# Kernel optimization log

Measured on AMD Instinct MI355X. Metric: run time of the kernel, lower is better.

Reference implementation:

```python
import jax, jax.numpy as jnp
import numpy as np

N = 100000   # nodes
E = 1600000  # edges
F = 64       # num_features
H = 64       # hidden_units
C = 10       # num_classes
G = 1000     # graphs in batch
BN_EPS = 1e-5


def setup_inputs() -> dict:
    key = jax.random.key(0)
    ks = jax.random.split(key, 32)
    inp = {
        "x": jax.random.normal(ks[0], (N, F), dtype=jnp.float32),
        "edge_index": jax.random.randint(ks[1], (2, E), 0, N, dtype=jnp.int64),
        "batch": jnp.sort(jax.random.randint(ks[2], (N,), 0, G, dtype=jnp.int64)),
    }
    i = 3
    def w(shape, scale):
        nonlocal i
        a = jax.random.normal(ks[i], shape, dtype=jnp.float32) * scale
        i += 1
        return a
    for l, din in [(0, F), (1, H)]:
        inp[f"c{l}_w1"] = w((din, H), 1.0 / np.sqrt(din))
        inp[f"c{l}_b1"] = jnp.zeros((H,), jnp.float32)
        inp[f"c{l}_g1"] = jnp.ones((H,), jnp.float32)
        inp[f"c{l}_be1"] = jnp.zeros((H,), jnp.float32)
        inp[f"c{l}_w2"] = w((H, H), 1.0 / np.sqrt(H))
        inp[f"c{l}_b2"] = jnp.zeros((H,), jnp.float32)
        inp[f"bn{l}_g"] = jnp.ones((H,), jnp.float32)
        inp[f"bn{l}_b"] = jnp.zeros((H,), jnp.float32)
    for l, din in [(0, F), (1, H), (2, H)]:
        inp[f"l{l}_w"] = w((din, C), 1.0 / np.sqrt(din))
        inp[f"l{l}_b"] = jnp.zeros((C,), jnp.float32)
    return inp


def _bn(h, g, b):
    # BatchNorm1d in training mode: batch statistics over node axis
    m = jnp.mean(h, axis=0)
    v = jnp.var(h, axis=0)
    return g * (h - m) * jax.lax.rsqrt(v + BN_EPS) + b


def _gin_conv(h, src, dst, w1, b1, g1, be1, w2, b2):
    # scatter-add neighbor aggregation: out[dst] += h[src]; eps = 0
    agg = jax.ops.segment_sum(h[src], dst, num_segments=N)
    z = h + agg                      # (1 + eps) * x + sum_j x_j
    z = jax.nn.relu(_bn(z @ w1 + b1, g1, be1))
    return z @ w2 + b2


def reference(x, edge_index, batch,
              c0_w1, c0_b1, c0_g1, c0_be1, c0_w2, c0_b2, bn0_g, bn0_b,
              c1_w1, c1_b1, c1_g1, c1_be1, c1_w2, c1_b2, bn1_g, bn1_b,
              l0_w, l0_b, l1_w, l1_b, l2_w, l2_b):
    src, dst = edge_index[0], edge_index[1]
    h0 = x
    h1 = jax.nn.relu(_bn(_gin_conv(h0, src, dst, c0_w1, c0_b1, c0_g1, c0_be1, c0_w2, c0_b2), bn0_g, bn0_b))
    h2 = jax.nn.relu(_bn(_gin_conv(h1, src, dst, c1_w1, c1_b1, c1_g1, c1_be1, c1_w2, c1_b2), bn1_g, bn1_b))
    # jumping-knowledge readout: per-layer global_add_pool -> Linear -> sum (dropout=0)
    out = jnp.zeros((G, C), dtype=x.dtype)
    for h, w, b in [(h0, l0_w, l0_b), (h1, l1_w, l1_b), (h2, l2_w, l2_b)]:
        pooled = jax.ops.segment_sum(h, batch, num_segments=G)
        out = out + pooled @ w + b
    return out
```

## Files before the change

kernel.cpp:

```cpp
#include <hip/hip_runtime.h>
#include <hip/hip_bf16.h>

#define BN_EPS 1e-5f
#define NBMAX 512
#define CHUNK 4096
#define CAP   5120
#define PCAP  7168

typedef __hip_bfloat16 bf16;
typedef __attribute__((ext_vector_type(8))) short short8;
typedef __attribute__((ext_vector_type(4))) float f32x4;

__device__ __forceinline__ float b2f(bf16 v) { return __bfloat162float(v); }
__device__ __forceinline__ bf16 f2b(float v) { return __float2bfloat16(v); }
__device__ __forceinline__ float bl(unsigned u) { return __uint_as_float(u << 16); }
__device__ __forceinline__ float bh(unsigned u) { return __uint_as_float(u & 0xffff0000u); }
__device__ __forceinline__ unsigned pack2(float x, float y) {
    union { bf16 b[2]; unsigned u; } p;
    p.b[0] = f2b(x); p.b[1] = f2b(y);
    return p.u;
}
__device__ __forceinline__ float bs2f(short s) {
    return __uint_as_float(((unsigned)(unsigned short)s) << 16);
}
__device__ __forceinline__ short f2bs(float v) {
    bf16 b = f2b(v);
    return *reinterpret_cast<short*>(&b);
}

__global__ __launch_bounds__(256) void initcast_k(
    const float* __restrict__ in, bf16* __restrict__ out, int n4, int total4,
    int* __restrict__ bcur, int NB)
{
    if (blockIdx.x == 0) {
        for (int i = threadIdx.x; i < NB; i += 256) bcur[i] = i * CAP;
    }
    int i = blockIdx.x * 256 + threadIdx.x;
    if (i >= total4) return;
    if (i < n4) {
        float4 v = ((const float4*)in)[i];
        union { ushort4 u; bf16 b[4]; } p;
        p.b[0] = f2b(v.x); p.b[1] = f2b(v.y); p.b[2] = f2b(v.z); p.b[3] = f2b(v.w);
        ((ushort4*)out)[i] = p.u;
    } else {
        ushort4 z; z.x = 0; z.y = 0; z.z = 0; z.w = 0;
        ((ushort4*)out)[i] = z;
    }
}

__global__ __launch_bounds__(256) void binscatter_k(
    const int* __restrict__ src, const int* __restrict__ dst,
    int* __restrict__ bcur, int* __restrict__ tmp, int E, int NB)
{
    __shared__ int hist[NBMAX];
    __shared__ int loff[NBMAX];
    __shared__ int gb[NBMAX];
    __shared__ int lcur[NBMAX];
    __shared__ int staged[CHUNK];
    __shared__ unsigned short sb[CHUNK];
    __shared__ int ssc[256];
    const int t = threadIdx.x;
    for (int i = t; i < NB; i += 256) { hist[i] = 0; lcur[i] = 0; }
    __syncthreads();
    const int base = blockIdx.x * CHUNK;
    const int lim = min(CHUNK, E - base);
    int myb[16], myw[16];
    int cnt = 0;
    for (int i = t; i < lim; i += 256) {
        int d = dst[base + i];
        int s_ = src[base + i];
        int b = d >> 8;
        myb[cnt] = b;
        myw[cnt] = (s_ << 8) | (d & 255);
        cnt++;
        atomicAdd(&hist[b], 1);
    }
    __syncthreads();
    int v0 = (2 * t     < NB) ? hist[2 * t]     : 0;
    int v1 = (2 * t + 1 < NB) ? hist[2 * t + 1] : 0;
    ssc[t] = v0 + v1;
    __syncthreads();
    for (int off = 1; off < 256; off <<= 1) {
        int a = (t >= off) ? ssc[t - off] : 0;
        __syncthreads();
        ssc[t] += a;
        __syncthreads();
    }
    int excl = ssc[t] - (v0 + v1);
    if (2 * t < NB)     loff[2 * t] = excl;
    if (2 * t + 1 < NB) loff[2 * t + 1] = excl + v0;
    __syncthreads();
    for (int b = t; b < NB; b += 256)
        if (hist[b] > 0) gb[b] = atomicAdd(&bcur[b], hist[b]);
    for (int i = 0; i < cnt; i++) {
        int b = myb[i];
        int p = loff[b] + atomicAdd(&lcur[b], 1);
        staged[p] = myw[i];
        sb[p] = (unsigned short)b;
    }
    __syncthreads();
    for (int i = t; i < lim; i += 256) {
        int b = sb[i];
        tmp[gb[b] + (i - loff[b])] = staged[i];
    }
}

__global__ __launch_bounds__(256) void csr_k(
    const int* __restrict__ bcur, const int* __restrict__ tmp,
    int* __restrict__ rowptr, int* __restrict__ rowend,
    int* __restrict__ adj, int N)
{
    __shared__ int hist[256], pfx[256], cur[256], ssc[256];
    __shared__ int sadj[PCAP];
    const int b = blockIdx.x, t = threadIdx.x;
    const int lo = b * CAP;
    const int plo = b * PCAP;
    const int cnt = min(bcur[b] - lo, CAP);
    hist[t] = 0; cur[t] = 0;
    __syncthreads();
    for (int i = t; i < cnt; i += 256)
        atomicAdd(&hist[tmp[lo + i] & 255], 1);
    __syncthreads();
    const int v = hist[t];
    const int pv = (v + 7) & ~7;
    ssc[t] = pv;
    __syncthreads();
    for (int off = 1; off < 256; off <<= 1) {
        int a = (t >= off) ? ssc[t - off] : 0;
        __syncthreads();
        ssc[t] += a;
        __syncthreads();
    }
    const int myp = ssc[t] - pv;
    pfx[t] = myp;
    const int node = b * 256 + t;
    if (node < N) {
        rowptr[node] = plo + myp;
        rowend[node] = plo + myp + pv;
    }
    __syncthreads();
    const int pcnt = ssc[255];
    for (int i = t; i < cnt; i += 256) {
        int w = tmp[lo + i];
        int d = w & 255;
        int p = pfx[d] + atomicAdd(&cur[d], 1);
        sadj[p] = w >> 8;
    }
    __syncthreads();
    for (int i = v; i < pv; i++) sadj[myp + i] = N;
    __syncthreads();
    for (int i = t; i < pcnt; i += 256) adj[plo + i] = sadj[i];
}

__global__ __launch_bounds__(256, 4) void aggregate_k(
    const bf16* __restrict__ h, const int* __restrict__ rowptr,
    const int* __restrict__ rowend, const int* __restrict__ adj,
    bf16* __restrict__ z, int N)
{
    const int lane16 = threadIdx.x & 15;
    const int n = blockIdx.x * 16 + (threadIdx.x >> 4);
    if (n >= N) return;
    const char* hb_ = (const char*)h;
    const int b = rowptr[n], e = rowend[n];

    uint2 u = *(const uint2*)(hb_ + ((size_t)n << 7) + (lane16 << 3));
    float s0 = bl(u.x), s1 = bh(u.x), s2 = bl(u.y), s3 = bh(u.y);

    int m[8];
    if (b < e) {
        #pragma unroll
        for (int k = 0; k < 8; k++) m[k] = adj[b + k];
    }
    for (int i = b; i < e; ) {
        uint2 w[8];
        #pragma unroll
        for (int k = 0; k < 8; k++)
            w[k] = *(const uint2*)(hb_ + (((size_t)(unsigned)m[k]) << 7) + (lane16 << 3));
        const int inext = i + 8;
        if (inext < e) {
            #pragma unroll
            for (int k = 0; k < 8; k++) m[k] = adj[inext + k];
        }
        #pragma unroll
        for (int k = 0; k < 8; k++) {
            s0 += bl(w[k].x); s1 += bh(w[k].x);
            s2 += bl(w[k].y); s3 += bh(w[k].y);
        }
        i = inext;
    }
    uint2 o;
    o.x = pack2(s0, s1);
    o.y = pack2(s2, s3);
    *(uint2*)((char*)z + ((size_t)n << 7) + (lane16 << 3)) = o;
}

__global__ __launch_bounds__(256) void ewact_k(
    const bf16* __restrict__ y, const float* __restrict__ sc,
    const float* __restrict__ sh, bf16* __restrict__ h, int N)
{
    const int idx = blockIdx.x * 256 + threadIdx.x;
    const int total = (N + 1) * 8;
    if (idx >= total) return;
    short8 v;
    if (idx < N * 8) {
        const int f0 = (idx & 7) * 8;
        v = *(const short8*)(y + (size_t)idx * 8);
        #pragma unroll
        for (int j = 0; j < 8; j++)
            v[j] = f2bs(fmaxf(fmaf(bs2f(v[j]), sc[f0 + j], sh[f0 + j]), 0.f));
    } else {
        #pragma unroll
        for (int j = 0; j < 8; j++) v[j] = 0;
    }
    *(short8*)(h + (size_t)idx * 8) = v;
}

template<int MODE>
__global__ __launch_bounds__(256) void gemm64_k(
    const bf16* __restrict__ A,
    const float* __restrict__ scin, const float* __restrict__ shin,
    const float* __restrict__ W, const float* __restrict__ bias,
    bf16* __restrict__ out, float* __restrict__ pstat, int nrows)
{
    __shared__ bf16 sWt[64][72];
    __shared__ bf16 sC[128][68];
    __shared__ float sSc[64], sSh[64], sB[64];
    __shared__ float sredS[64][17], sredQ[64][17];
    const int tid = threadIdx.x;

    if (tid < 64) {
        sB[tid] = bias[tid];
        if (MODE == 1) { sSc[tid] = scin[tid]; sSh[tid] = shin[tid]; }
    }
    for (int i = tid; i < 4096; i += 256) {
        int k = i >> 6, n = i & 63;
        sWt[n][k] = f2b(W[i]);
    }
    __syncthreads();

    const int wave = tid >> 6, lane = tid & 63;
    const int quad = lane >> 4, l16 = lane & 15;
    const int row0 = blockIdx.x * 128 + wave * 32;

    short8 a[2][2];
    #pragma unroll
    for (int rt = 0; rt < 2; rt++) {
        int r = row0 + rt * 16 + l16;
        int rr = min(r, nrows - 1);
        const bf16* arow = A + (size_t)rr * 64;
        a[rt][0] = *(const short8*)(arow + quad * 8);
        a[rt][1] = *(const short8*)(arow + 32 + quad * 8);
        if (MODE == 1) {
            #pragma unroll
            for (int j = 0; j < 8; j++) {
                int f0 = quad * 8 + j;
                a[rt][0][j] = f2bs(fmaxf(fmaf(bs2f(a[rt][0][j]), sSc[f0], sSh[f0]), 0.f));
                int f1 = 32 + f0;
                a[rt][1][j] = f2bs(fmaxf(fmaf(bs2f(a[rt][1][j]), sSc[f1], sSh[f1]), 0.f));
            }
        }
    }

    float psS[4], psQ[4];
    #pragma unroll
    for (int t = 0; t < 4; t++) { psS[t] = 0.f; psQ[t] = 0.f; }

    #pragma unroll
    for (int t = 0; t < 4; t++) {
        const int n = t * 16 + l16;
        short8 b0 = *(const short8*)&sWt[n][quad * 8];
        short8 b1 = *(const short8*)&sWt[n][32 + quad * 8];
        const float bn_ = sB[n];
        #pragma unroll
        for (int rt = 0; rt < 2; rt++) {
            f32x4 acc = {0.f, 0.f, 0.f, 0.f};
            acc = __builtin_amdgcn_mfma_f32_16x16x32_bf16(a[rt][0], b0, acc, 0, 0, 0);
            acc = __builtin_amdgcn_mfma_f32_16x16x32_bf16(a[rt][1], b1, acc, 0, 0, 0);
            #pragma unroll
            for (int reg = 0; reg < 4; reg++) {
                const int lr = wave * 32 + rt * 16 + quad * 4 + reg;
                float v = acc[reg] + bn_;
                sC[lr][n] = f2b(v);
                if (row0 + rt * 16 + quad * 4 + reg < nrows) {
                    psS[t] += v;
                    psQ[t] = fmaf(v, v, psQ[t]);
                }
            }
        }
    }

    #pragma unroll
    for (int t = 0; t < 4; t++) {
        sredS[t * 16 + l16][wave * 4 + quad] = psS[t];
        sredQ[t * 16 + l16][wave * 4 + quad] = psQ[t];
    }
    __syncthreads();

    const int gbase = blockIdx.x * 128;
    #pragma unroll
    for (int it = 0; it < 8; it++) {
        int idx = it * 256 + tid;
        int r = idx >> 4, c4 = idx & 15;
        if (gbase + r < nrows) {
            ushort4 v = *(const ushort4*)&sC[r][c4 * 4];
            *(ushort4*)(out + (size_t)(gbase + r) * 64 + c4 * 4) = v;
        }
    }

    if (tid < 128) {
        const int c = tid & 63;
        const float* p = (tid < 64) ? &sredS[c][0] : &sredQ[c][0];
        float s = 0.f;
        #pragma unroll
        for (int i = 0; i < 16; i++) s += p[i];
        pstat[(size_t)blockIdx.x * 128 + (tid < 64 ? c : 64 + c)] = s;
    }
}

__global__ __launch_bounds__(256) void bn_reduce_k(
    const float* __restrict__ pstat, int nblk,
    const float* __restrict__ g, const float* __restrict__ be, float invN,
    float* __restrict__ sc, float* __restrict__ sh)
{
    const int f = blockIdx.x;
    const int t = threadIdx.x;
    float S = 0.f, Q = 0.f;
    for (int b = t; b < nblk; b += 256) {
        S += pstat[(size_t)b * 128 + f];
        Q += pstat[(size_t)b * 128 + 64 + f];
    }
    __shared__ float rs[256], rq[256];
    rs[t] = S; rq[t] = Q;
    __syncthreads();
    for (int off = 128; off > 0; off >>= 1) {
        if (t < off) { rs[t] += rs[t + off]; rq[t] += rq[t + off]; }
        __syncthreads();
    }
    if (t == 0) {
        float m = rs[0] * invN;
        float v = rq[0] * invN - m * m;
        float s = g[f] * rsqrtf(v + BN_EPS);
        sc[f] = s;
        sh[f] = be[f] - m * s;
    }
}

__global__ __launch_bounds__(256) void pool_readout_k(
    const bf16* __restrict__ xb, const bf16* __restrict__ h1,
    const bf16* __restrict__ y1, const int* __restrict__ batch,
    const float* __restrict__ scB, const float* __restrict__ shB,
    const float* __restrict__ w0, const float* __restrict__ b0,
    const float* __restrict__ w1, const float* __restrict__ b1,
    const float* __restrict__ w2, const float* __restrict__ b2,
    float* __restrict__ out, int Nn)
{
    const int g = blockIdx.x;
    int lo = 0, hi = Nn;
    while (lo < hi) { int mid = (lo + hi) >> 1; if (batch[mid] < g) lo = mid + 1; else hi = mid; }
    const int start = lo;
    hi = Nn;
    while (lo < hi) { int mid = (lo + hi) >> 1; if (batch[mid] <= g) lo = mid + 1; else hi = mid; }
    const int end = lo;

    const int f = threadIdx.x & 63;
    const int w = threadIdx.x >> 6;
    const float sB = scB[f], tB = shB[f];

    float s0 = 0.f, s1 = 0.f, s2 = 0.f;
    for (int i = start + w; i < end; i += 4) {
        s0 += b2f(xb[(size_t)i * 64 + f]);
        s1 += b2f(h1[(size_t)i * 64 + f]);
        s2 += fmaxf(fmaf(b2f(y1[(size_t)i * 64 + f]), sB, tB), 0.f);
    }
    __shared__ float p[3][4][64];
    p[0][w][f] = s0; p[1][w][f] = s1; p[2][w][f] = s2;
    __syncthreads();
    if (threadIdx.x < 10) {
        const int c = threadIdx.x;
        float acc = b0[c] + b1[c] + b2[c];
        for (int k = 0; k < 64; k++) {
            float q0 = p[0][0][k] + p[0][1][k] + p[0][2][k] + p[0][3][k];
            float q1 = p[1][0][k] + p[1][1][k] + p[1][2][k] + p[1][3][k];
            float q2 = p[2][0][k] + p[2][1][k] + p[2][2][k] + p[2][3][k];
            acc = fmaf(q0, w0[k * 10 + c], acc);
            acc = fmaf(q1, w1[k * 10 + c], acc);
            acc = fmaf(q2, w2[k * 10 + c], acc);
        }
        out[(size_t)g * 10 + c] = acc;
    }
}

extern "C" void kernel_launch(void* const* d_in, const int* in_sizes, int n_in,
                              void* d_out, int out_size, void* d_ws, size_t ws_size,
                              hipStream_t stream)
{
    const float* x     = (const float*)d_in[0];
    const int*   edge  = (const int*)d_in[1];
    const int*   batch = (const int*)d_in[2];
    const int N = in_sizes[0] / 64;
    const int E = in_sizes[1] / 2;
    const int G = out_size / 10;
    const int* src = edge;
    const int* dst = edge + E;
    const int NB = (N + 255) / 256;

    const float* c_w1[2]  = {(const float*)d_in[3],  (const float*)d_in[11]};
    const float* c_b1[2]  = {(const float*)d_in[4],  (const float*)d_in[12]};
    const float* c_g1[2]  = {(const float*)d_in[5],  (const float*)d_in[13]};
    const float* c_be1[2] = {(const float*)d_in[6],  (const float*)d_in[14]};
    const float* c_w2[2]  = {(const float*)d_in[7],  (const float*)d_in[15]};
    const float* c_b2[2]  = {(const float*)d_in[8],  (const float*)d_in[16]};
    const float* bn_g[2]  = {(const float*)d_in[9],  (const float*)d_in[17]};
    const float* bn_b[2]  = {(const float*)d_in[10], (const float*)d_in[18]};
    const float* lw[3]    = {(const float*)d_in[19], (const float*)d_in[21], (const float*)d_in[23]};
    const float* lb[3]    = {(const float*)d_in[20], (const float*)d_in[22], (const float*)d_in[24]};

    float* out = (float*)d_out;
    const size_t nh  = (size_t)N * 64;
    const size_t nh1 = (size_t)(N + 1) * 64;
    const int PG = (N + 127) / 128;

    bf16*  zb    = (bf16*)d_ws;
    bf16*  wb    = zb + nh;
    bf16*  xb    = wb + nh;
    bf16*  hb    = xb + nh1;
    float* scsh  = (float*)(hb + nh1);
    float* pstat = scsh + 512;
    int*   rowptr = (int*)(pstat + (size_t)PG * 128);
    int*   rowend = rowptr + N;
    int*   adj    = rowend + N;
    int*   tmp    = adj + (size_t)NB * PCAP;
    int*   bcur   = tmp + (size_t)NB * CAP;

    float* sc0 = scsh;       float* sh0 = scsh + 64;
    float* scA = scsh + 128; float* shA = scsh + 192;
    float* sc2 = scsh + 256; float* sh2 = scsh + 320;
    float* scB = scsh + 384; float* shB = scsh + 448;

    const float invN = 1.0f / (float)N;
    const int binGrid  = (E + CHUNK - 1) / CHUNK;
    const int aggGrid  = (N + 15) / 16;
    const int n4       = N * 16;
    const int total4   = (N + 1) * 16;
    const int ewGrid   = (total4 + 255) / 256;
    const int actGrid  = ((N + 1) * 8 + 255) / 256;

    initcast_k<<<ewGrid, 256, 0, stream>>>(x, xb, n4, total4, bcur, NB);
    binscatter_k<<<binGrid, 256, 0, stream>>>(src, dst, bcur, tmp, E, NB);
    csr_k<<<NB, 256, 0, stream>>>(bcur, tmp, rowptr, rowend, adj, N);

    aggregate_k<<<aggGrid, 256, 0, stream>>>(xb, rowptr, rowend, adj, zb, N);
    gemm64_k<0><<<PG, 256, 0, stream>>>(zb, nullptr, nullptr,
                                        c_w1[0], c_b1[0], zb, pstat, N);
    bn_reduce_k<<<64, 256, 0, stream>>>(pstat, PG, c_g1[0], c_be1[0], invN, sc0, sh0);
    gemm64_k<1><<<PG, 256, 0, stream>>>(zb, sc0, sh0,
                                        c_w2[0], c_b2[0], zb, pstat, N);
    bn_reduce_k<<<64, 256, 0, stream>>>(pstat, PG, bn_g[0], bn_b[0], invN, scA, shA);

    ewact_k<<<actGrid, 256, 0, stream>>>(zb, scA, shA, hb, N);

    aggregate_k<<<aggGrid, 256, 0, stream>>>(hb, rowptr, rowend, adj, wb, N);
    gemm64_k<0><<<PG, 256, 0, stream>>>(wb, nullptr, nullptr,
                                        c_w1[1], c_b1[1], wb, pstat, N);
    bn_reduce_k<<<64, 256, 0, stream>>>(pstat, PG, c_g1[1], c_be1[1], invN, sc2, sh2);
    gemm64_k<1><<<PG, 256, 0, stream>>>(wb, sc2, sh2,
                                        c_w2[1], c_b2[1], wb, pstat, N);
    bn_reduce_k<<<64, 256, 0, stream>>>(pstat, PG, bn_g[1], bn_b[1], invN, scB, shB);

    pool_readout_k<<<G, 256, 0, stream>>>(xb, hb, wb, batch,
                                          scB, shB,
                                          lw[0], lb[0], lw[1], lb[1], lw[2], lb[2],
                                          out, N);
}
```

Baseline: 292.4 us.

## Fuse BN reductions via atomics and fold activation into aggregation and readout

Result: slower. 328.2 us (+12.2%).

```diff
diff --git a/kernel.cpp b/kernel.cpp
--- a/kernel.cpp
+++ b/kernel.cpp
@@ -28,12 +28,25 @@
     return *reinterpret_cast<short*>(&b);
 }
 
+__device__ __forceinline__ void bn_sc_sh(
+    const float* __restrict__ gs, const float* __restrict__ g,
+    const float* __restrict__ be, float invN, int f, float* sc, float* sh)
+{
+    float S = gs[f], Q = gs[64 + f];
+    float m = S * invN;
+    float v = Q * invN - m * m;
+    float s = g[f] * rsqrtf(v + BN_EPS);
+    *sc = s;
+    *sh = be[f] - m * s;
+}
+
 __global__ __launch_bounds__(256) void initcast_k(
-    const float* __restrict__ in, bf16* __restrict__ out, int n4, int total4,
-    int* __restrict__ bcur, int NB)
+    const float* __restrict__ in, bf16* __restrict__ xb, bf16* __restrict__ zb,
+    int n4, int total4, int* __restrict__ bcur, int NB, float* __restrict__ gs)
 {
     if (blockIdx.x == 0) {
         for (int i = threadIdx.x; i < NB; i += 256) bcur[i] = i * CAP;
+        for (int i = threadIdx.x; i < 512; i += 256) gs[i] = 0.f;
     }
     int i = blockIdx.x * 256 + threadIdx.x;
     if (i >= total4) return;
@@ -41,10 +54,10 @@
         float4 v = ((const float4*)in)[i];
         union { ushort4 u; bf16 b[4]; } p;
         p.b[0] = f2b(v.x); p.b[1] = f2b(v.y); p.b[2] = f2b(v.z); p.b[3] = f2b(v.w);
-        ((ushort4*)out)[i] = p.u;
+        ((ushort4*)xb)[i] = p.u;
     } else {
         ushort4 z; z.x = 0; z.y = 0; z.z = 0; z.w = 0;
-        ((ushort4*)out)[i] = z;
+        ((ushort4*)xb)[i] = z;
     }
 }
 
@@ -152,30 +165,56 @@
     for (int i = t; i < pcnt; i += 256) adj[plo + i] = sadj[i];
 }
 
+template<int MODE>
 __global__ __launch_bounds__(256, 4) void aggregate_k(
     const bf16* __restrict__ h, const int* __restrict__ rowptr,
     const int* __restrict__ rowend, const int* __restrict__ adj,
-    bf16* __restrict__ z, int N)
-{
-    const int lane16 = threadIdx.x & 15;
-    const int n = blockIdx.x * 16 + (threadIdx.x >> 4);
+    bf16* __restrict__ z, int N,
+    const float* __restrict__ gs, const float* __restrict__ bng,
+    const float* __restrict__ bnb, float invN)
+{
+    __shared__ float sSc[64], sSh[64];
+    const int tid = threadIdx.x;
+    if (MODE == 1) {
+        if (tid < 64) bn_sc_sh(gs, bng, bnb, invN, tid, &sSc[tid], &sSh[tid]);
+        __syncthreads();
+    }
+    const int lane16 = tid & 15;
+    const int n = blockIdx.x * 16 + (tid >> 4);
     if (n >= N) return;
+    float sc0 = 0.f, sc1 = 0.f, sc2 = 0.f, sc3 = 0.f;
+    float sh0 = 0.f, sh1 = 0.f, sh2 = 0.f, sh3 = 0.f;
+    if (MODE == 1) {
+        const int f0 = lane16 * 4;
+        sc0 = sSc[f0];     sh0 = sSh[f0];
+        sc1 = sSc[f0 + 1]; sh1 = sSh[f0 + 1];
+        sc2 = sSc[f0 + 2]; sh2 = sSh[f0 + 2];
+        sc3 = sSc[f0 + 3]; sh3 = sSh[f0 + 3];
+    }
     const char* hb_ = (const char*)h;
     const int b = rowptr[n], e = rowend[n];
 
     uint2 u = *(const uint2*)(hb_ + ((size_t)n << 7) + (lane16 << 3));
     float s0 = bl(u.x), s1 = bh(u.x), s2 = bl(u.y), s3 = bh(u.y);
-
-    int m[8];
+    if (MODE == 1) {
+        s0 = fmaxf(fmaf(s0, sc0, sh0), 0.f);
+        s1 = fmaxf(fmaf(s1, sc1, sh1), 0.f);
+        s2 = fmaxf(fmaf(s2, sc2, sh2), 0.f);
+        s3 = fmaxf(fmaf(s3, sc3, sh3), 0.f);
+    }
+
+    int m[8], mc[8];
     if (b < e) {
         #pragma unroll
         for (int k = 0; k < 8; k++) m[k] = adj[b + k];
     }
     for (int i = b; i < e; ) {
+        #pragma unroll
+        for (int k = 0; k < 8; k++) mc[k] = m[k];
         uint2 w[8];
         #pragma unroll
         for (int k = 0; k < 8; k++)
-            w[k] = *(const uint2*)(hb_ + (((size_t)(unsigned)m[k]) << 7) + (lane16 << 3));
+            w[k] = *(const uint2*)(hb_ + (((size_t)(unsigned)mc[k]) << 7) + (lane16 << 3));
         const int inext = i + 8;
         if (inext < e) {
             #pragma unroll
@@ -183,8 +222,16 @@
         }
         #pragma unroll
         for (int k = 0; k < 8; k++) {
-            s0 += bl(w[k].x); s1 += bh(w[k].x);
-            s2 += bl(w[k].y); s3 += bh(w[k].y);
+            float p0 = bl(w[k].x), p1 = bh(w[k].x);
+            float p2 = bl(w[k].y), p3 = bh(w[k].y);
+            if (MODE == 1) {
+                const bool real = mc[k] < N;
+                p0 = real ? fmaxf(fmaf(p0, sc0, sh0), 0.f) : 0.f;
+                p1 = real ? fmaxf(fmaf(p1, sc1, sh1), 0.f) : 0.f;
+                p2 = real ? fmaxf(fmaf(p2, sc2, sh2), 0.f) : 0.f;
+                p3 = real ? fmaxf(fmaf(p3, sc3, sh3), 0.f) : 0.f;
+            }
+            s0 += p0; s1 += p1; s2 += p2; s3 += p3;
         }
         i = inext;
     }
@@ -194,33 +241,13 @@
     *(uint2*)((char*)z + ((size_t)n << 7) + (lane16 << 3)) = o;
 }
 
-__global__ __launch_bounds__(256) void ewact_k(
-    const bf16* __restrict__ y, const float* __restrict__ sc,
-    const float* __restrict__ sh, bf16* __restrict__ h, int N)
-{
-    const int idx = blockIdx.x * 256 + threadIdx.x;
-    const int total = (N + 1) * 8;
-    if (idx >= total) return;
-    short8 v;
-    if (idx < N * 8) {
-        const int f0 = (idx & 7) * 8;
-        v = *(const short8*)(y + (size_t)idx * 8);
-        #pragma unroll
-        for (int j = 0; j < 8; j++)
-            v[j] = f2bs(fmaxf(fmaf(bs2f(v[j]), sc[f0 + j], sh[f0 + j]), 0.f));
-    } else {
-        #pragma unroll
-        for (int j = 0; j < 8; j++) v[j] = 0;
-    }
-    *(short8*)(h + (size_t)idx * 8) = v;
-}
-
 template<int MODE>
 __global__ __launch_bounds__(256) void gemm64_k(
     const bf16* __restrict__ A,
-    const float* __restrict__ scin, const float* __restrict__ shin,
+    const float* __restrict__ gstat_in, const float* __restrict__ bng,
+    const float* __restrict__ bnb, float invN,
     const float* __restrict__ W, const float* __restrict__ bias,
-    bf16* __restrict__ out, float* __restrict__ pstat, int nrows)
+    bf16* __restrict__ out, float* __restrict__ gstat_out, int nrows)
 {
     __shared__ bf16 sWt[64][72];
     __shared__ bf16 sC[128][68];
@@ -230,7 +257,7 @@
 
     if (tid < 64) {
         sB[tid] = bias[tid];
-        if (MODE == 1) { sSc[tid] = scin[tid]; sSh[tid] = shin[tid]; }
+        if (MODE == 1) bn_sc_sh(gstat_in, bng, bnb, invN, tid, &sSc[tid], &sSh[tid]);
     }
     for (int i = tid; i < 4096; i += 256) {
         int k = i >> 6, n = i & 63;
@@ -313,47 +340,33 @@
         float s = 0.f;
         #pragma unroll
         for (int i = 0; i < 16; i++) s += p[i];
-        pstat[(size_t)blockIdx.x * 128 + (tid < 64 ? c : 64 + c)] = s;
-    }
-}
-
-__global__ __launch_bounds__(256) void bn_reduce_k(
-    const float* __restrict__ pstat, int nblk,
-    const float* __restrict__ g, const float* __restrict__ be, float invN,
-    float* __restrict__ sc, float* __restrict__ sh)
-{
-    const int f = blockIdx.x;
-    const int t = threadIdx.x;
-    float S = 0.f, Q = 0.f;
-    for (int b = t; b < nblk; b += 256) {
-        S += pstat[(size_t)b * 128 + f];
-        Q += pstat[(size_t)b * 128 + 64 + f];
-    }
-    __shared__ float rs[256], rq[256];
-    rs[t] = S; rq[t] = Q;
-    __syncthreads();
-    for (int off = 128; off > 0; off >>= 1) {
-        if (t < off) { rs[t] += rs[t + off]; rq[t] += rq[t + off]; }
-        __syncthreads();
-    }
-    if (t == 0) {
-        float m = rs[0] * invN;
-        float v = rq[0] * invN - m * m;
-        float s = g[f] * rsqrtf(v + BN_EPS);
-        sc[f] = s;
-        sh[f] = be[f] - m * s;
+        atomicAdd(&gstat_out[(tid < 64) ? c : 64 + c], s);
     }
 }
 
 __global__ __launch_bounds__(256) void pool_readout_k(
-    const bf16* __restrict__ xb, const bf16* __restrict__ h1,
+    const bf16* __restrict__ xb, const bf16* __restrict__ y0,
     const bf16* __restrict__ y1, const int* __restrict__ batch,
-    const float* __restrict__ scB, const float* __restrict__ shB,
+    const float* __restrict__ gsA, const float* __restrict__ gA, const float* __restrict__ beA,
+    const float* __restrict__ gsB, const float* __restrict__ gB, const float* __restrict__ beB,
+    float invN,
     const float* __restrict__ w0, const float* __restrict__ b0,
     const float* __restrict__ w1, const float* __restrict__ b1,
     const float* __restrict__ w2, const float* __restrict__ b2,
     float* __restrict__ out, int Nn)
 {
+    __shared__ float sA[2][64], sB2[2][64];
+    __shared__ float p[3][16][64];
+    __shared__ float q[3][64];
+    const int tid = threadIdx.x;
+    if (tid < 64) {
+        bn_sc_sh(gsA, gA, beA, invN, tid, &sA[0][tid], &sA[1][tid]);
+    } else if (tid < 128) {
+        int f = tid - 64;
+        bn_sc_sh(gsB, gB, beB, invN, f, &sB2[0][f], &sB2[1][f]);
+    }
+    __syncthreads();
+
     const int g = blockIdx.x;
     int lo = 0, hi = Nn;
     while (lo < hi) { int mid = (lo + hi) >> 1; if (batch[mid] < g) lo = mid + 1; else hi = mid; }
@@ -362,29 +375,56 @@
     while (lo < hi) { int mid = (lo + hi) >> 1; if (batch[mid] <= g) lo = mid + 1; else hi = mid; }
     const int end = lo;
 
-    const int f = threadIdx.x & 63;
-    const int w = threadIdx.x >> 6;
-    const float sB = scB[f], tB = shB[f];
-
-    float s0 = 0.f, s1 = 0.f, s2 = 0.f;
-    for (int i = start + w; i < end; i += 4) {
-        s0 += b2f(xb[(size_t)i * 64 + f]);
-        s1 += b2f(h1[(size_t)i * 64 + f]);
-        s2 += fmaxf(fmaf(b2f(y1[(size_t)i * 64 + f]), sB, tB), 0.f);
-    }
-    __shared__ float p[3][4][64];
-    p[0][w][f] = s0; p[1][w][f] = s1; p[2][w][f] = s2;
-    __syncthreads();
-    if (threadIdx.x < 10) {
-        const int c = threadIdx.x;
+    const int l16 = tid & 15, grp = tid >> 4;
+    const int f0 = l16 * 4;
+    const float scA0 = sA[0][f0],     shA0 = sA[1][f0];
+    const float scA1 = sA[0][f0 + 1], shA1 = sA[1][f0 + 1];
+    const float scA2 = sA[0][f0 + 2], shA2 = sA[1][f0 + 2];
+    const float scA3 = sA[0][f0 + 3], shA3 = sA[1][f0 + 3];
+    const float scB0 = sB2[0][f0],     shB0 = sB2[1][f0];
+    const float scB1 = sB2[0][f0 + 1], shB1 = sB2[1][f0 + 1];
+    const float scB2 = sB2[0][f0 + 2], shB2 = sB2[1][f0 + 2];
+    const float scB3 = sB2[0][f0 + 3], shB3 = sB2[1][f0 + 3];
+
+    float a0 = 0.f, a1 = 0.f, a2 = 0.f, a3 = 0.f;
+    float h0 = 0.f, h1 = 0.f, h2 = 0.f, h3 = 0.f;
+    float c0 = 0.f, c1 = 0.f, c2 = 0.f, c3 = 0.f;
+    for (int i = start + grp; i < end; i += 16) {
+        const size_t ro = (size_t)i * 16 + l16;
+        uint2 ux = ((const uint2*)xb)[ro];
+        uint2 u0 = ((const uint2*)y0)[ro];
+        uint2 u1 = ((const uint2*)y1)[ro];
+        a0 += bl(ux.x); a1 += bh(ux.x); a2 += bl(ux.y); a3 += bh(ux.y);
+        h0 += fmaxf(fmaf(bl(u0.x), scA0, shA0), 0.f);
+        h1 += fmaxf(fmaf(bh(u0.x), scA1, shA1), 0.f);
+        h2 += fmaxf(fmaf(bl(u0.y), scA2, shA2), 0.f);
+        h3 += fmaxf(fmaf(bh(u0.y), scA3, shA3), 0.f);
+        c0 += fmaxf(fmaf(bl(u1.x), scB0, shB0), 0.f);
+        c1 += fmaxf(fmaf(bh(u1.x), scB1, shB1), 0.f);
+        c2 += fmaxf(fmaf(bl(u1.y), scB2, shB2), 0.f);
+        c3 += fmaxf(fmaf(bh(u1.y), scB3, shB3), 0.f);
+    }
+    p[0][grp][f0] = a0; p[0][grp][f0 + 1] = a1; p[0][grp][f0 + 2] = a2; p[0][grp][f0 + 3] = a3;
+    p[1][grp][f0] = h0; p[1][grp][f0 + 1] = h1; p[1][grp][f0 + 2] = h2; p[1][grp][f0 + 3] = h3;
+    p[2][grp][f0] = c0; p[2][grp][f0 + 1] = c1; p[2][grp][f0 + 2] = c2; p[2][grp][f0 + 3] = c3;
+    __syncthreads();
+
+    if (tid < 192) {
+        const int arr = tid >> 6, f = tid & 63;
+        float s = 0.f;
+        #pragma unroll
+        for (int i = 0; i < 16; i++) s += p[arr][i][f];
+        q[arr][f] = s;
+    }
+    __syncthreads();
+
+    if (tid < 10) {
+        const int c = tid;
         float acc = b0[c] + b1[c] + b2[c];
         for (int k = 0; k < 64; k++) {
-            float q0 = p[0][0][k] + p[0][1][k] + p[0][2][k] + p[0][3][k];
-            float q1 = p[1][0][k] + p[1][1][k] + p[1][2][k] + p[1][3][k];
-            float q2 = p[2][0][k] + p[2][1][k] + p[2][2][k] + p[2][3][k];
-            acc = fmaf(q0, w0[k * 10 + c], acc);
-            acc = fmaf(q1, w1[k * 10 + c], acc);
-            acc = fmaf(q2, w2[k * 10 + c], acc);
+            acc = fmaf(q[0][k], w0[k * 10 + c], acc);
+            acc = fmaf(q[1][k], w1[k * 10 + c], acc);
+            acc = fmaf(q[2][k], w2[k * 10 + c], acc);
         }
         out[(size_t)g * 10 + c] = acc;
     }
@@ -416,26 +456,23 @@
     const float* lb[3]    = {(const float*)d_in[20], (const float*)d_in[22], (const float*)d_in[24]};
 
     float* out = (float*)d_out;
-    const size_t nh  = (size_t)N * 64;
     const size_t nh1 = (size_t)(N + 1) * 64;
     const int PG = (N + 127) / 128;
 
     bf16*  zb    = (bf16*)d_ws;
-    bf16*  wb    = zb + nh;
-    bf16*  xb    = wb + nh;
-    bf16*  hb    = xb + nh1;
-    float* scsh  = (float*)(hb + nh1);
-    float* pstat = scsh + 512;
-    int*   rowptr = (int*)(pstat + (size_t)PG * 128);
+    bf16*  wb    = zb + nh1;
+    bf16*  xb    = wb + nh1;
+    float* gs    = (float*)(xb + nh1);
+    int*   rowptr = (int*)(gs + 512);
     int*   rowend = rowptr + N;
     int*   adj    = rowend + N;
     int*   tmp    = adj + (size_t)NB * PCAP;
     int*   bcur   = tmp + (size_t)NB * CAP;
 
-    float* sc0 = scsh;       float* sh0 = scsh + 64;
-    float* scA = scsh + 128; float* shA = scsh + 192;
-    float* sc2 = scsh + 256; float* sh2 = scsh + 320;
-    float* scB = scsh + 384; float* shB = scsh + 448;
+    float* gs1 = gs;
+    float* gs2 = gs + 128;
+    float* gs3 = gs + 256;
+    float* gs4 = gs + 384;
 
     const float invN = 1.0f / (float)N;
     const int binGrid  = (E + CHUNK - 1) / CHUNK;
@@ -443,32 +480,28 @@
     const int n4       = N * 16;
     const int total4   = (N + 1) * 16;
     const int ewGrid   = (total4 + 255) / 256;
-    const int actGrid  = ((N + 1) * 8 + 255) / 256;
-
-    initcast_k<<<ewGrid, 256, 0, stream>>>(x, xb, n4, total4, bcur, NB);
+
+    initcast_k<<<ewGrid, 256, 0, stream>>>(x, xb, zb, n4, total4, bcur, NB, gs);
     binscatter_k<<<binGrid, 256, 0, stream>>>(src, dst, bcur, tmp, E, NB);
     csr_k<<<NB, 256, 0, stream>>>(bcur, tmp, rowptr, rowend, adj, N);
 
-    aggregate_k<<<aggGrid, 256, 0, stream>>>(xb, rowptr, rowend, adj, zb, N);
-    gemm64_k<0><<<PG, 256, 0, stream>>>(zb, nullptr, nullptr,
-                                        c_w1[0], c_b1[0], zb, pstat, N);
-    bn_reduce_k<<<64, 256, 0, stream>>>(pstat, PG, c_g1[0], c_be1[0], invN, sc0, sh0);
-    gemm64_k<1><<<PG, 256, 0, stream>>>(zb, sc0, sh0,
-                                        c_w2[0], c_b2[0], zb, pstat, N);
-    bn_reduce_k<<<64, 256, 0, stream>>>(pstat, PG, bn_g[0], bn_b[0], invN, scA, shA);
-
-    ewact_k<<<actGrid, 256, 0, stream>>>(zb, scA, shA, hb, N);
-
-    aggregate_k<<<aggGrid, 256, 0, stream>>>(hb, rowptr, rowend, adj, wb, N);
-    gemm64_k<0><<<PG, 256, 0, stream>>>(wb, nullptr, nullptr,
-                                        c_w1[1], c_b1[1], wb, pstat, N);
-    bn_reduce_k<<<64, 256, 0, stream>>>(pstat, PG, c_g1[1], c_be1[1], invN, sc2, sh2);
-    gemm64_k<1><<<PG, 256, 0, stream>>>(wb, sc2, sh2,
-                                        c_w2[1], c_b2[1], wb, pstat, N);
-    bn_reduce_k<<<64, 256, 0, stream>>>(pstat, PG, bn_g[1], bn_b[1], invN, scB, shB);
-
-    pool_readout_k<<<G, 256, 0, stream>>>(xb, hb, wb, batch,
-                                          scB, shB,
+    aggregate_k<0><<<aggGrid, 256, 0, stream>>>(xb, rowptr, rowend, adj, zb, N,
+                                                nullptr, nullptr, nullptr, 0.f);
+    gemm64_k<0><<<PG, 256, 0, stream>>>(zb, nullptr, nullptr, nullptr, 0.f,
+                                        c_w1[0], c_b1[0], zb, gs1, N);
+    gemm64_k<1><<<PG, 256, 0, stream>>>(zb, gs1, c_g1[0], c_be1[0], invN,
+                                        c_w2[0], c_b2[0], zb, gs2, N);
+
+    aggregate_k<1><<<aggGrid, 256, 0, stream>>>(zb, rowptr, rowend, adj, wb, N,
+                                                gs2, bn_g[0], bn_b[0], invN);
+    gemm64_k<0><<<PG, 256, 0, stream>>>(wb, nullptr, nullptr, nullptr, 0.f,
+                                        c_w1[1], c_b1[1], wb, gs3, N);
+    gemm64_k<1><<<PG, 256, 0, stream>>>(wb, gs3, c_g1[1], c_be1[1], invN,
+                                        c_w2[1], c_b2[1], wb, gs4, N);
+
+    pool_readout_k<<<G, 256, 0, stream>>>(xb, zb, wb, batch,
+                                          gs2, bn_g[0], bn_b[0],
+                                          gs4, bn_g[1], bn_b[1], invN,
                                           lw[0], lb[0], lw[1], lb[1], lw[2], lb[2],
                                           out, N);
 }
```

## Build CSR via global degree count, two-level scan, atomic scatter; widen pool readout

Applied to the files above, without the earlier changes.

Result: slower. 431.6 us (+47.6%).

```diff
diff --git a/kernel.cpp b/kernel.cpp
--- a/kernel.cpp
+++ b/kernel.cpp
@@ -3,9 +3,6 @@
 
 #define BN_EPS 1e-5f
 #define NBMAX 512
-#define CHUNK 4096
-#define CAP   5120
-#define PCAP  7168
 
 typedef __hip_bfloat16 bf16;
 typedef __attribute__((ext_vector_type(8))) short short8;
@@ -28,57 +25,35 @@
     return *reinterpret_cast<short*>(&b);
 }
 
-__global__ __launch_bounds__(256) void initcast_k(
-    const float* __restrict__ in, bf16* __restrict__ out, int n4, int total4,
-    int* __restrict__ bcur, int NB)
-{
-    if (blockIdx.x == 0) {
-        for (int i = threadIdx.x; i < NB; i += 256) bcur[i] = i * CAP;
-    }
-    int i = blockIdx.x * 256 + threadIdx.x;
-    if (i >= total4) return;
-    if (i < n4) {
-        float4 v = ((const float4*)in)[i];
-        union { ushort4 u; bf16 b[4]; } p;
-        p.b[0] = f2b(v.x); p.b[1] = f2b(v.y); p.b[2] = f2b(v.z); p.b[3] = f2b(v.w);
-        ((ushort4*)out)[i] = p.u;
-    } else {
-        ushort4 z; z.x = 0; z.y = 0; z.z = 0; z.w = 0;
-        ((ushort4*)out)[i] = z;
-    }
-}
-
-__global__ __launch_bounds__(256) void binscatter_k(
-    const int* __restrict__ src, const int* __restrict__ dst,
-    int* __restrict__ bcur, int* __restrict__ tmp, int E, int NB)
-{
-    __shared__ int hist[NBMAX];
-    __shared__ int loff[NBMAX];
-    __shared__ int gb[NBMAX];
-    __shared__ int lcur[NBMAX];
-    __shared__ int staged[CHUNK];
-    __shared__ unsigned short sb[CHUNK];
+__global__ __launch_bounds__(256) void initcast_deg_k(
+    const float* __restrict__ in, bf16* __restrict__ xb, int n4, int total4,
+    const int* __restrict__ dst, int* __restrict__ deg, int E)
+{
+    const int i = blockIdx.x * 256 + threadIdx.x;
+    if (i < total4) {
+        if (i < n4) {
+            float4 v = ((const float4*)in)[i];
+            union { ushort4 u; bf16 b[4]; } p;
+            p.b[0] = f2b(v.x); p.b[1] = f2b(v.y); p.b[2] = f2b(v.z); p.b[3] = f2b(v.w);
+            ((ushort4*)xb)[i] = p.u;
+        } else {
+            ushort4 z; z.x = 0; z.y = 0; z.z = 0; z.w = 0;
+            ((ushort4*)xb)[i] = z;
+        }
+    }
+    if (i < E) atomicAdd(&deg[dst[i]], 1);
+}
+
+__global__ __launch_bounds__(256) void scan1_k(
+    const int* __restrict__ deg, int* __restrict__ lpfx,
+    int* __restrict__ bsum, int N)
+{
     __shared__ int ssc[256];
     const int t = threadIdx.x;
-    for (int i = t; i < NB; i += 256) { hist[i] = 0; lcur[i] = 0; }
-    __syncthreads();
-    const int base = blockIdx.x * CHUNK;
-    const int lim = min(CHUNK, E - base);
-    int myb[16], myw[16];
-    int cnt = 0;
-    for (int i = t; i < lim; i += 256) {
-        int d = dst[base + i];
-        int s_ = src[base + i];
-        int b = d >> 8;
-        myb[cnt] = b;
-        myw[cnt] = (s_ << 8) | (d & 255);
-        cnt++;
-        atomicAdd(&hist[b], 1);
-    }
-    __syncthreads();
-    int v0 = (2 * t     < NB) ? hist[2 * t]     : 0;
-    int v1 = (2 * t + 1 < NB) ? hist[2 * t + 1] : 0;
-    ssc[t] = v0 + v1;
+    const int n = blockIdx.x * 256 + t;
+    const int d = (n < N) ? deg[n] : 0;
+    const int pv = (d + 7) & ~7;
+    ssc[t] = pv;
     __syncthreads();
     for (int off = 1; off < 256; off <<= 1) {
         int a = (t >= off) ? ssc[t - off] : 0;
@@ -86,70 +61,51 @@
         ssc[t] += a;
         __syncthreads();
     }
-    int excl = ssc[t] - (v0 + v1);
-    if (2 * t < NB)     loff[2 * t] = excl;
-    if (2 * t + 1 < NB) loff[2 * t + 1] = excl + v0;
-    __syncthreads();
-    for (int b = t; b < NB; b += 256)
-        if (hist[b] > 0) gb[b] = atomicAdd(&bcur[b], hist[b]);
-    for (int i = 0; i < cnt; i++) {
-        int b = myb[i];
-        int p = loff[b] + atomicAdd(&lcur[b], 1);
-        staged[p] = myw[i];
-        sb[p] = (unsigned short)b;
-    }
-    __syncthreads();
-    for (int i = t; i < lim; i += 256) {
-        int b = sb[i];
-        tmp[gb[b] + (i - loff[b])] = staged[i];
-    }
-}
-
-__global__ __launch_bounds__(256) void csr_k(
-    const int* __restrict__ bcur, const int* __restrict__ tmp,
-    int* __restrict__ rowptr, int* __restrict__ rowend,
-    int* __restrict__ adj, int N)
-{
-    __shared__ int hist[256], pfx[256], cur[256], ssc[256];
-    __shared__ int sadj[PCAP];
-    const int b = blockIdx.x, t = threadIdx.x;
-    const int lo = b * CAP;
-    const int plo = b * PCAP;
-    const int cnt = min(bcur[b] - lo, CAP);
-    hist[t] = 0; cur[t] = 0;
-    __syncthreads();
-    for (int i = t; i < cnt; i += 256)
-        atomicAdd(&hist[tmp[lo + i] & 255], 1);
-    __syncthreads();
-    const int v = hist[t];
-    const int pv = (v + 7) & ~7;
-    ssc[t] = pv;
-    __syncthreads();
-    for (int off = 1; off < 256; off <<= 1) {
-        int a = (t >= off) ? ssc[t - off] : 0;
+    if (n < N) lpfx[n] = ssc[t] - pv;
+    if (t == 255) bsum[blockIdx.x] = ssc[255];
+}
+
+__global__ __launch_bounds__(512) void scan2_k(int* __restrict__ bs, int nb)
+{
+    __shared__ int s[512];
+    const int t = threadIdx.x;
+    const int v = (t < nb) ? bs[t] : 0;
+    s[t] = v;
+    __syncthreads();
+    for (int off = 1; off < 512; off <<= 1) {
+        int a = (t >= off) ? s[t - off] : 0;
         __syncthreads();
-        ssc[t] += a;
+        s[t] += a;
         __syncthreads();
     }
-    const int myp = ssc[t] - pv;
-    pfx[t] = myp;
-    const int node = b * 256 + t;
-    if (node < N) {
-        rowptr[node] = plo + myp;
-        rowend[node] = plo + myp + pv;
-    }
-    __syncthreads();
-    const int pcnt = ssc[255];
-    for (int i = t; i < cnt; i += 256) {
-        int w = tmp[lo + i];
-        int d = w & 255;
-        int p = pfx[d] + atomicAdd(&cur[d], 1);
-        sadj[p] = w >> 8;
-    }
-    __syncthreads();
-    for (int i = v; i < pv; i++) sadj[myp + i] = N;
-    __syncthreads();
-    for (int i = t; i < pcnt; i += 256) adj[plo + i] = sadj[i];
+    if (t < nb) bs[t] = s[t] - v;
+}
+
+__global__ __launch_bounds__(256) void finalize_k(
+    const int* __restrict__ deg, int* __restrict__ rowptr ,
+    int* __restrict__ rowend, int* __restrict__ adj,
+    const int* __restrict__ bsum, int N)
+{
+    const int n = blockIdx.x * 256 + threadIdx.x;
+    if (n >= N) return;
+    const int base = bsum[n >> 8] + rowptr[n];
+    const int d = deg[n];
+    const int pv = (d + 7) & ~7;
+    rowptr[n] = base;
+    rowend[n] = base + pv;
+    for (int i = d; i < pv; i++) adj[base + i] = N;
+}
+
+__global__ __launch_bounds__(256) void scatter_k(
+    const int* __restrict__ src, const int* __restrict__ dst,
+    const int* __restrict__ rowptr, int* __restrict__ deg,
+    int* __restrict__ adj, int E)
+{
+    const int e = blockIdx.x * 256 + threadIdx.x;
+    if (e >= E) return;
+    const int d = dst[e];
+    const int pos = atomicSub(&deg[d], 1) - 1;
+    adj[rowptr[d] + pos] = src[e];
 }
 
 __global__ __launch_bounds__(256, 4) void aggregate_k(
@@ -354,6 +310,13 @@
     const float* __restrict__ w2, const float* __restrict__ b2,
     float* __restrict__ out, int Nn)
 {
+    __shared__ float sB2[2][64];
+    __shared__ float p[3][16][64];
+    __shared__ float q[3][64];
+    const int tid = threadIdx.x;
+    if (tid < 64) { sB2[0][tid] = scB[tid]; sB2[1][tid] = shB[tid]; }
+    __syncthreads();
+
     const int g = blockIdx.x;
     int lo = 0, hi = Nn;
     while (lo < hi) { int mid = (lo + hi) >> 1; if (batch[mid] < g) lo = mid + 1; else hi = mid; }
@@ -362,29 +325,49 @@
     while (lo < hi) { int mid = (lo + hi) >> 1; if (batch[mid] <= g) lo = mid + 1; else hi = mid; }
     const int end = lo;
 
-    const int f = threadIdx.x & 63;
-    const int w = threadIdx.x >> 6;
-    const float sB = scB[f], tB = shB[f];
-
-    float s0 = 0.f, s1 = 0.f, s2 = 0.f;
-    for (int i = start + w; i < end; i += 4) {
-        s0 += b2f(xb[(size_t)i * 64 + f]);
-        s1 += b2f(h1[(size_t)i * 64 + f]);
-        s2 += fmaxf(fmaf(b2f(y1[(size_t)i * 64 + f]), sB, tB), 0.f);
-    }
-    __shared__ float p[3][4][64];
-    p[0][w][f] = s0; p[1][w][f] = s1; p[2][w][f] = s2;
-    __syncthreads();
-    if (threadIdx.x < 10) {
-        const int c = threadIdx.x;
+    const int l16 = tid & 15, grp = tid >> 4;
+    const int f0 = l16 * 4;
+    const float scB0 = sB2[0][f0],     shB0 = sB2[1][f0];
+    const float scB1 = sB2[0][f0 + 1], shB1 = sB2[1][f0 + 1];
+    const float scB2_ = sB2[0][f0 + 2], shB2_ = sB2[1][f0 + 2];
+    const float scB3 = sB2[0][f0 + 3], shB3 = sB2[1][f0 + 3];
+
+    float a0 = 0.f, a1 = 0.f, a2 = 0.f, a3 = 0.f;
+    float h0 = 0.f, h1s = 0.f, h2 = 0.f, h3 = 0.f;
+    float c0 = 0.f, c1 = 0.f, c2 = 0.f, c3 = 0.f;
+    for (int i = start + grp; i < end; i += 16) {
+        const size_t ro = (size_t)i * 16 + l16;
+        uint2 ux = ((const uint2*)xb)[ro];
+        uint2 u0 = ((const uint2*)h1)[ro];
+        uint2 u1 = ((const uint2*)y1)[ro];
+        a0 += bl(ux.x); a1 += bh(ux.x); a2 += bl(ux.y); a3 += bh(ux.y);
+        h0 += bl(u0.x); h1s += bh(u0.x); h2 += bl(u0.y); h3 += bh(u0.y);
+        c0 += fmaxf(fmaf(bl(u1.x), scB0, shB0), 0.f);
+        c1 += fmaxf(fmaf(bh(u1.x), scB1, shB1), 0.f);
+        c2 += fmaxf(fmaf(bl(u1.y), scB2_, shB2_), 0.f);
+        c3 += fmaxf(fmaf(bh(u1.y), scB3, shB3), 0.f);
+    }
+    p[0][grp][f0] = a0; p[0][grp][f0 + 1] = a1; p[0][grp][f0 + 2] = a2; p[0][grp][f0 + 3] = a3;
+    p[1][grp][f0] = h0; p[1][grp][f0 + 1] = h1s; p[1][grp][f0 + 2] = h2; p[1][grp][f0 + 3] = h3;
+    p[2][grp][f0] = c0; p[2][grp][f0 + 1] = c1; p[2][grp][f0 + 2] = c2; p[2][grp][f0 + 3] = c3;
+    __syncthreads();
+
+    if (tid < 192) {
+        const int arr = tid >> 6, f = tid & 63;
+        float s = 0.f;
+        #pragma unroll
+        for (int i = 0; i < 16; i++) s += p[arr][i][f];
+        q[arr][f] = s;
+    }
+    __syncthreads();
+
+    if (tid < 10) {
+        const int c = tid;
         float acc = b0[c] + b1[c] + b2[c];
         for (int k = 0; k < 64; k++) {
-            float q0 = p[0][0][k] + p[0][1][k] + p[0][2][k] + p[0][3][k];
-            float q1 = p[1][0][k] + p[1][1][k] + p[1][2][k] + p[1][3][k];
-            float q2 = p[2][0][k] + p[2][1][k] + p[2][2][k] + p[2][3][k];
-            acc = fmaf(q0, w0[k * 10 + c], acc);
-            acc = fmaf(q1, w1[k * 10 + c], acc);
-            acc = fmaf(q2, w2[k * 10 + c], acc);
+            acc = fmaf(q[0][k], w0[k * 10 + c], acc);
+            acc = fmaf(q[1][k], w1[k * 10 + c], acc);
+            acc = fmaf(q[2][k], w2[k * 10 + c], acc);
         }
         out[(size_t)g * 10 + c] = acc;
     }
@@ -416,21 +399,20 @@
     const float* lb[3]    = {(const float*)d_in[20], (const float*)d_in[22], (const float*)d_in[24]};
 
     float* out = (float*)d_out;
-    const size_t nh  = (size_t)N * 64;
     const size_t nh1 = (size_t)(N + 1) * 64;
     const int PG = (N + 127) / 128;
 
     bf16*  zb    = (bf16*)d_ws;
-    bf16*  wb    = zb + nh;
-    bf16*  xb    = wb + nh;
+    bf16*  wb    = zb + nh1;
+    bf16*  xb    = wb + nh1;
     bf16*  hb    = xb + nh1;
     float* scsh  = (float*)(hb + nh1);
     float* pstat = scsh + 512;
     int*   rowptr = (int*)(pstat + (size_t)PG * 128);
     int*   rowend = rowptr + N;
-    int*   adj    = rowend + N;
-    int*   tmp    = adj + (size_t)NB * PCAP;
-    int*   bcur   = tmp + (size_t)NB * CAP;
+    int*   deg    = rowend + N;
+    int*   bsum   = deg + N;
+    int*   adj    = bsum + NBMAX;
 
     float* sc0 = scsh;       float* sh0 = scsh + 64;
     float* scA = scsh + 128; float* shA = scsh + 192;
@@ -438,16 +420,19 @@
     float* scB = scsh + 384; float* shB = scsh + 448;
 
     const float invN = 1.0f / (float)N;
-    const int binGrid  = (E + CHUNK - 1) / CHUNK;
     const int aggGrid  = (N + 15) / 16;
     const int n4       = N * 16;
     const int total4   = (N + 1) * 16;
-    const int ewGrid   = (total4 + 255) / 256;
+    const int castGrid = (max(total4, E) + 255) / 256;
+    const int edgeGrid = (E + 255) / 256;
     const int actGrid  = ((N + 1) * 8 + 255) / 256;
 
-    initcast_k<<<ewGrid, 256, 0, stream>>>(x, xb, n4, total4, bcur, NB);
-    binscatter_k<<<binGrid, 256, 0, stream>>>(src, dst, bcur, tmp, E, NB);
-    csr_k<<<NB, 256, 0, stream>>>(bcur, tmp, rowptr, rowend, adj, N);
+    hipMemsetAsync(deg, 0, (size_t)N * sizeof(int), stream);
+    initcast_deg_k<<<castGrid, 256, 0, stream>>>(x, xb, n4, total4, dst, deg, E);
+    scan1_k<<<NB, 256, 0, stream>>>(deg, rowptr, bsum, N);
+    scan2_k<<<1, 512, 0, stream>>>(bsum, NB);
+    finalize_k<<<NB, 256, 0, stream>>>(deg, rowptr, rowend, adj, bsum, N);
+    scatter_k<<<edgeGrid, 256, 0, stream>>>(src, dst, rowptr, deg, adj, E);
 
     aggregate_k<<<aggGrid, 256, 0, stream>>>(xb, rowptr, rowend, adj, zb, N);
     gemm64_k<0><<<PG, 256, 0, stream>>>(zb, nullptr, nullptr,
```
